# Performance work log

Measured on AMD Instinct MI355X. Metric: run time of the kernel, lower is better.

The kernel has to match this reference:

```python
import jax, jax.numpy as jnp
import numpy as np
import math

B, T, F_ = 4, 1024, 1024
TO_DIM, FROM_DIM, LATENT, H = 1024, 1024, 1024, 16
HEAD_DIM = LATENT // H

def _linear_params(key, in_dim, out_dim):
    kw, kb = jax.random.split(key)
    bound = 1.0 / math.sqrt(in_dim)
    W = jax.random.uniform(kw, (out_dim, in_dim), minval=-bound, maxval=bound, dtype=jnp.float32)
    b = jax.random.uniform(kb, (out_dim,), minval=-bound, maxval=bound, dtype=jnp.float32)
    return W, b

def setup_inputs() -> dict:
    key = jax.random.key(0)
    ks = jax.random.split(key, 7)
    X_to = jax.random.normal(ks[0], (B, T, TO_DIM), dtype=jnp.float32)
    X_from = jax.random.normal(ks[1], (B, F_, FROM_DIM), dtype=jnp.float32)
    mask_from = jax.random.randint(ks[2], (B, T, F_), 0, 2, dtype=jnp.int32)
    Wq, bq = _linear_params(ks[3], TO_DIM, LATENT)
    Wk, bk = _linear_params(ks[4], FROM_DIM, LATENT)
    Wv, bv = _linear_params(ks[5], FROM_DIM, LATENT)
    Wo, bo = _linear_params(ks[6], LATENT, TO_DIM)
    return {"X_to": X_to, "X_from": X_from, "mask_from": mask_from,
            "Wq": Wq, "bq": bq, "Wk": Wk, "bk": bk, "Wv": Wv, "bv": bv, "Wo": Wo, "bo": bo}

def _split_heads(x):
    # [b, t, (h k)] -> [b, h, t, k]
    b, t, _ = x.shape
    return x.reshape(b, t, H, HEAD_DIM).transpose(0, 2, 1, 3)

def reference(X_to, X_from, mask_from, Wq, bq, Wk, bk, Wv, bv, Wo, bo):
    Q = _split_heads(X_to @ Wq.T + bq)
    # NOTE: source swaps names — K comes from v_linear, V from k_linear. Reproduced literally.
    K = _split_heads(X_from @ Wv.T + bv)
    V = _split_heads(X_from @ Wk.T + bk)
    attn = jnp.einsum('bhtk,bhfk->bhtf', Q, K) / math.sqrt(HEAD_DIM)
    attn = jnp.where(mask_from[:, None, :, :] == 0, jnp.float32(-10000.0), attn)
    attn = jax.nn.softmax(attn, axis=-1)
    out = jnp.einsum('bhtf,bhfk->bhtk', attn, V)  # [b,h,t,k]
    out = out.transpose(0, 2, 1, 3).reshape(X_to.shape[0], X_to.shape[1], LATENT)
    return out @ Wo.T + bo
```

## Files before the change

### kernel.cpp

```cpp
#include <hip/hip_runtime.h>
#include <hip/hip_bf16.h>
#include <math.h>

#define BB 4
#define TT 1024
#define FF 1024
#define DIM 1024
#define NH 16
#define HD 64
#define MROWS (BB * TT)
#define FB (FF / 64)

typedef __attribute__((ext_vector_type(8))) short short8;
typedef __attribute__((ext_vector_type(4))) short short4v;
typedef __attribute__((ext_vector_type(4))) float f32x4;
typedef __hip_bfloat16 bf16;

__device__ __forceinline__ void async_copy16(const void* g, void* l) {
    __builtin_amdgcn_global_load_lds((const __attribute__((address_space(1))) void*)g,
                                     (__attribute__((address_space(3))) void*)l,
                                     16, 0, 0);
}

struct ConvArgs {
    const float* src[6];
    bf16* dst[6];
    int nvec[6];
    int blk_end[6];
    const int* mask;
    unsigned long long* Mb;
};

__global__ __launch_bounds__(256) void convert_pack(ConvArgs a) {
    int bx = blockIdx.x;
    if (bx >= a.blk_end[5]) {
        const int lane = threadIdx.x & 63;
        const int waveId = (bx - a.blk_end[5]) * 4 + (threadIdx.x >> 6);
#pragma unroll
        for (int it = 0; it < 16; ++it) {
            int c = waveId * 16 + it;
            int v = a.mask[(size_t)c * 64 + lane];
            unsigned long long bits = __ballot(v != 0);
            if (lane == 0) a.Mb[c] = bits;
        }
        return;
    }
    int seg = 0;
#pragma unroll
    for (int k = 0; k < 5; ++k) if (bx >= a.blk_end[k]) seg = k + 1;
    int b0 = seg ? a.blk_end[seg - 1] : 0;
    int idx = (bx - b0) * 256 + threadIdx.x;
    if (idx >= a.nvec[seg]) return;
    float4 v = ((const float4*)a.src[seg])[idx];
    union { bf16 t[4]; ushort4 u; } o;
    o.t[0] = __float2bfloat16(v.x);
    o.t[1] = __float2bfloat16(v.y);
    o.t[2] = __float2bfloat16(v.z);
    o.t[3] = __float2bfloat16(v.w);
    *(ushort4*)(a.dst[seg] + 4 * (size_t)idx) = o.u;
}

#define BK 64

struct QkvArgs {
    const bf16* A[3]; const bf16* W[3]; const float* bias[3]; bf16* C[3];
    int N[3]; int biasRow[3]; float scale[3];
};

#define BARRIER() __builtin_amdgcn_s_barrier()

__global__ __launch_bounds__(512) void gemm_qkv(QkvArgs q) {
    __shared__ bf16 lds[67584];

    const int op = blockIdx.y;
    const bf16* A = q.A[op];
    const bf16* W = q.W[op];
    const float* bias = q.bias[op];
    bf16* C = q.C[op];
    const int N = q.N[op];
    const int brow = q.biasRow[op];
    const float sc = q.scale[op];

    const int lin = blockIdx.x;
    const int xcd = lin & 7;
    const int t8  = lin >> 3;
    int mt, nt;
    if (brow) { mt = t8 & 3; nt = xcd * 2 + (t8 >> 2); }
    else      { mt = xcd * 2 + (t8 >> 2); nt = t8 & 3; }
    const int m0 = mt * 256, n0 = nt * 256;

    const int tid  = threadIdx.x;
    const int lane = tid & 63;
    const int wave = tid >> 6;
    const int quad = lane >> 4;
    const int l16  = lane & 15;
    const int wm   = wave >> 2;
    const int wn   = wave & 3;
    const int wbase = tid & ~63;

    const int srow = tid >> 3;
    const int scol = (tid & 7) ^ (srow & 7);
    const bf16* pA = A + (size_t)(m0 + srow) * DIM + scol * 8;
    const bf16* pB = W + (size_t)(n0 + srow) * DIM + scol * 8;

#define STAGE(P, ISB, TTL, HH) do { \
    const bf16* s_ = (P) + (size_t)(HH) * (128 * DIM) + (TTL) * 64; \
    bf16* d_ = lds + ((TTL) & 1) * 32768 + (ISB) * 16384 + (HH) * 8192 + wbase * 8; \
    async_copy16(s_, d_); \
    async_copy16(s_ + 64 * DIM, d_ + 4096); \
} while (0)

    f32x4 acc[8][4] = {};
    short8 a[4][2], b[4][2];

    STAGE(pA, 0, 0, 0); STAGE(pB, 1, 0, 0);
    STAGE(pA, 0, 0, 1); STAGE(pB, 1, 0, 1);
    STAGE(pA, 0, 1, 0); STAGE(pB, 1, 1, 0);
    asm volatile("s_waitcnt vmcnt(4)");
    BARRIER();

#define LDA(AH) do { \
    _Pragma("unroll") for (int miq = 0; miq < 4; ++miq) { \
        int r_ = (AH) * 128 + wm * 64 + miq * 16 + l16; \
        const bf16* ba_ = Ab + r_ * 64; \
        a[miq][0] = *(const short8*)(ba_ + ((quad ^ (r_ & 7)) * 8)); \
        a[miq][1] = *(const short8*)(ba_ + (((quad + 4) ^ (r_ & 7)) * 8)); \
    } } while (0)

#define LDB(BH) do { \
    _Pragma("unroll") for (int niq = 0; niq < 2; ++niq) { \
        int r_ = (BH) * 128 + wn * 32 + niq * 16 + l16; \
        const bf16* bb_ = Bb + r_ * 64; \
        b[(BH) * 2 + niq][0] = *(const short8*)(bb_ + ((quad ^ (r_ & 7)) * 8)); \
        b[(BH) * 2 + niq][1] = *(const short8*)(bb_ + (((quad + 4) ^ (r_ & 7)) * 8)); \
    } } while (0)

#define MMA(AH, BH) do { \
    _Pragma("unroll") for (int miq = 0; miq < 4; ++miq) \
    _Pragma("unroll") for (int niq = 0; niq < 2; ++niq) { \
        f32x4& c_ = acc[(AH) * 4 + miq][(BH) * 2 + niq]; \
        c_ = __builtin_amdgcn_mfma_f32_16x16x32_bf16(a[miq][0], b[(BH) * 2 + niq][0], c_, 0, 0, 0); \
        c_ = __builtin_amdgcn_mfma_f32_16x16x32_bf16(a[miq][1], b[(BH) * 2 + niq][1], c_, 0, 0, 0); \
    } } while (0)

#define PHASE_MFMA(AH, BH) do { \
    BARRIER(); \
    __builtin_amdgcn_s_setprio(1); \
    MMA(AH, BH); \
    __builtin_amdgcn_s_setprio(0); \
} while (0)

#pragma unroll 2
    for (int t = 0; t < 16; ++t) {
        const bf16* Ab = lds + (t & 1) * 32768;
        const bf16* Bb = Ab + 16384;

        LDA(0); LDB(0);
        if (t + 1 < 16) STAGE(pA, 0, t + 1, 1);
        PHASE_MFMA(0, 0);
        BARRIER();

        LDB(1);
        if (t + 1 < 16) STAGE(pB, 1, t + 1, 1);
        PHASE_MFMA(0, 1);
        BARRIER();

        LDA(1);
        if (t + 2 < 16) STAGE(pA, 0, t + 2, 0);
        PHASE_MFMA(1, 0);
        BARRIER();

        if (t + 2 < 16) STAGE(pB, 1, t + 2, 0);
        PHASE_MFMA(1, 1);
        if (t < 14)       { asm volatile("s_waitcnt vmcnt(4)"); }
        else if (t == 14) { asm volatile("s_waitcnt vmcnt(0)"); }
        BARRIER();
    }

    bf16* Cs = lds;
#pragma unroll
    for (int ni = 0; ni < 4; ++ni) {
        const int nl = (ni >> 1) * 128 + wn * 32 + (ni & 1) * 16 + l16;
        float bcol = brow ? 0.0f : bias[n0 + nl];
#pragma unroll
        for (int mi = 0; mi < 8; ++mi)
#pragma unroll
            for (int i = 0; i < 4; ++i) {
                const int ml = (mi >> 2) * 128 + wm * 64 + (mi & 3) * 16 + quad * 4 + i;
                float v = (acc[mi][ni][i] + (brow ? bias[m0 + ml] : bcol)) * sc;
                Cs[ml * 264 + nl] = __float2bfloat16(v);
            }
    }
    __syncthreads();
#pragma unroll
    for (int j = 0; j < 16; ++j) {
        int slot = j * 512 + tid;
        int rr = slot >> 5, cc = slot & 31;
        short8 v = *(const short8*)(Cs + rr * 264 + cc * 8);
        *(short8*)(C + (size_t)(m0 + rr) * N + n0 + cc * 8) = v;
    }
#undef STAGE
#undef LDA
#undef LDB
#undef MMA
#undef PHASE_MFMA
}

__global__ __launch_bounds__(256) void gemm_o(
    const bf16* __restrict__ A, const bf16* __restrict__ W,
    const float* __restrict__ bias, float* __restrict__ C)
{
    __shared__ float smemf[128 * 66];
    bf16* As = (bf16*)smemf;
    bf16* Bs = As + 128 * BK;

    const int lin = blockIdx.x + 16 * blockIdx.y;
    const int xcd = lin & 7;
    const int t   = lin >> 3;
    const int m0 = (xcd * 4 + (t >> 4)) * 128;
    const int n0 = (((t & 15) + 2 * xcd) & 15) * 64;

    const int tid  = threadIdx.x;
    const int lane = tid & 63;
    const int wave = tid >> 6;
    const int quad = lane >> 4;
    const int l16  = lane & 15;
    const int wm = wave & 1;
    const int wn = wave >> 1;
    const int wbase = tid & ~63;

    f32x4 acc[4][2] = {};

    for (int k0 = 0; k0 < DIM; k0 += BK) {
#pragma unroll
        for (int j = 0; j < 4; ++j) {
            int slot = j * 256 + tid;
            int r = slot >> 3;
            int g = (slot & 7) ^ (r & 7);
            async_copy16(A + (size_t)(m0 + r) * DIM + k0 + g * 8,
                         As + (size_t)(j * 256 + wbase) * 8);
        }
#pragma unroll
        for (int j = 0; j < 2; ++j) {
            int slot = j * 256 + tid;
            int r = slot >> 3;
            int g = (slot & 7) ^ (r & 7);
            async_copy16(W + (size_t)(n0 + r) * DIM + k0 + g * 8,
                         Bs + (size_t)(j * 256 + wbase) * 8);
        }
        __syncthreads();

#pragma unroll
        for (int kk = 0; kk < 2; ++kk) {
            short8 a[4], b[2];
#pragma unroll
            for (int mi = 0; mi < 4; ++mi) {
                int r = wm * 64 + mi * 16 + l16;
                int p = (kk * 4 + quad) ^ (r & 7);
                a[mi] = *(const short8*)(As + r * BK + p * 8);
            }
#pragma unroll
            for (int ni = 0; ni < 2; ++ni) {
                int r = wn * 32 + ni * 16 + l16;
                int p = (kk * 4 + quad) ^ (r & 7);
                b[ni] = *(const short8*)(Bs + r * BK + p * 8);
            }
#pragma unroll
            for (int mi = 0; mi < 4; ++mi)
#pragma unroll
                for (int ni = 0; ni < 2; ++ni)
                    acc[mi][ni] = __builtin_amdgcn_mfma_f32_16x16x32_bf16(
                        a[mi], b[ni], acc[mi][ni], 0, 0, 0);
        }
        __syncthreads();
    }

    float* Cs = smemf;
#pragma unroll
    for (int ni = 0; ni < 2; ++ni) {
        const int nl = wn * 32 + ni * 16 + l16;
        const float bcol = bias[n0 + nl];
#pragma unroll
        for (int mi = 0; mi < 4; ++mi)
#pragma unroll
            for (int i = 0; i < 4; ++i) {
                const int ml = wm * 64 + mi * 16 + quad * 4 + i;
                Cs[ml * 66 + nl] = acc[mi][ni][i] + bcol;
            }
    }
    __syncthreads();
#pragma unroll
    for (int j = 0; j < 8; ++j) {
        int slot = j * 256 + tid;
        int rr = slot >> 4, cc = slot & 15;
        float4 v = *(const float4*)(Cs + rr * 66 + cc * 4);
        *(float4*)(C + (size_t)(m0 + rr) * DIM + n0 + cc * 4) = v;
    }
}

__global__ __launch_bounds__(256, 3) void attn_kernel(
    const bf16* Qg, const bf16* __restrict__ Kg, const bf16* __restrict__ Vtg,
    const unsigned long long* __restrict__ Mbits, bf16* Og)
{
    __shared__ bf16 Ks[2 * 64 * 64];
    __shared__ bf16 Vts[2 * 64 * 64];
    __shared__ bf16 Pt[64 * 72];
    __shared__ float ls[64];

    const int tid  = threadIdx.x;
    const int lane = tid & 63;
    const int wave = tid >> 6;
    const int quad = lane >> 4;
    const int l16  = lane & 15;

    const int lin = blockIdx.x + 16 * (blockIdx.y + 16 * blockIdx.z);
    const int xcd = lin & 7;
    const int t   = lin >> 3;
    const int bh  = xcd * 8 + (t >> 4);
    const int b   = bh >> 4;
    const int h   = bh & 15;
    const int t0  = (t & 15) * 64;

    const size_t qrow0 = (size_t)b * TT + t0;
    const size_t krow0 = (size_t)b * FF;
    const int wbase = tid & ~63;
    const int myrow = wave * 16 + l16;

    const bf16* qptr = Qg + (qrow0 + myrow) * DIM + h * HD;
    short8 qb0 = *(const short8*)(qptr + quad * 8);
    short8 qb1 = *(const short8*)(qptr + 32 + quad * 8);

    const int srow = tid >> 3;
    const int sg   = ((tid & 7) ^ (srow & 7)) * 8;
    const bf16* kS = Kg + (krow0 + srow) * DIM + h * HD + sg;
    const bf16* vS = Vtg + (size_t)(h * HD + srow) * MROWS + b * FF + sg;

#define STAGE_KV(BUF, IT) do { \
    const bf16* ks_ = kS + (size_t)((IT) * 64) * DIM; \
    const bf16* vs_ = vS + (IT) * 64; \
    bf16* kd_ = Ks + (BUF) * 4096 + wbase * 8; \
    bf16* vd_ = Vts + (BUF) * 4096 + wbase * 8; \
    async_copy16(ks_, kd_); \
    async_copy16(ks_ + (size_t)32 * DIM, kd_ + 2048); \
    async_copy16(vs_, vd_); \
    async_copy16(vs_ + (size_t)32 * MROWS, vd_ + 2048); \
} while (0)

    const unsigned long long* mrow = Mbits + (qrow0 + myrow) * FB;
    unsigned long long w = mrow[0];

    float lsum = 0.f;
    f32x4 oacc[4] = {};

    STAGE_KV(0, 0);
    STAGE_KV(1, 1);
    asm volatile("s_waitcnt vmcnt(4)");
    BARRIER();

#pragma unroll 2
    for (int it = 0; it < 16; ++it) {
        const bf16* Kc = Ks + (it & 1) * 4096;
        const bf16* Vc = Vts + (it & 1) * 4096;

        unsigned long long nw = (it < 15) ? mrow[it + 1] : 0;

        f32x4 sacc[4];
        __builtin_amdgcn_s_setprio(1);
#pragma unroll
        for (int ft = 0; ft < 4; ++ft) {
            int r = ft * 16 + l16;
            short8 ka0 = *(const short8*)(Kc + r * 64 + ((quad       ^ (r & 7)) * 8));
            short8 ka1 = *(const short8*)(Kc + r * 64 + (((quad + 4) ^ (r & 7)) * 8));
            f32x4 s = {};
            s = __builtin_amdgcn_mfma_f32_16x16x32_bf16(ka0, qb0, s, 0, 0, 0);
            s = __builtin_amdgcn_mfma_f32_16x16x32_bf16(ka1, qb1, s, 0, 0, 0);
            sacc[ft] = s;
        }
        __builtin_amdgcn_s_setprio(0);

#pragma unroll
        for (int ft = 0; ft < 4; ++ft) {
            const unsigned bits4 =
                (unsigned)(w >> (ft * 16 + quad * 4)) & 0xFu;
            union { short4v v; short s[4]; } pk;
            float psum = 0.f;
#pragma unroll
            for (int i = 0; i < 4; ++i) {
                float p = (bits4 >> i) & 1u ? __expf(sacc[ft][i]) : 0.f;
                psum += p;
                pk.s[i] = (short)__bfloat16_as_ushort(__float2bfloat16(p));
            }
            lsum += psum;
            *(short4v*)(Pt + myrow * 72 + ft * 16 + quad * 4) = pk.v;
        }
        w = nw;

        short8 pa[2];
        pa[0] = *(const short8*)(Pt + myrow * 72 + quad * 8);
        pa[1] = *(const short8*)(Pt + myrow * 72 + 32 + quad * 8);
        __builtin_amdgcn_s_setprio(1);
#pragma unroll
        for (int nt = 0; nt < 4; ++nt) {
            int rd = nt * 16 + l16;
#pragma unroll
            for (int kf = 0; kf < 2; ++kf) {
                int g = (kf * 4 + quad) ^ (rd & 7);
                short8 vb = *(const short8*)(Vc + rd * 64 + g * 8);
                oacc[nt] = __builtin_amdgcn_mfma_f32_16x16x32_bf16(pa[kf], vb, oacc[nt], 0, 0, 0);
            }
        }
        __builtin_amdgcn_s_setprio(0);

        BARRIER();
        if (it + 2 < 16) STAGE_KV(it & 1, it + 2);
        if (it < 14)       { asm volatile("s_waitcnt vmcnt(4)"); }
        else if (it == 14) { asm volatile("s_waitcnt vmcnt(0)"); }
        BARRIER();
    }
#undef STAGE_KV

    lsum += __shfl_xor(lsum, 16);
    lsum += __shfl_xor(lsum, 32);
    if (quad == 0) ls[myrow] = lsum;

#pragma unroll
    for (int i = 0; i < 4; ++i) {
        float inv = 1.0f / ls[wave * 16 + quad * 4 + i];
        const int prow = wave * 16 + quad * 4 + i;
#pragma unroll
        for (int nt = 0; nt < 4; ++nt)
            Pt[prow * 72 + nt * 16 + l16] = __float2bfloat16(oacc[nt][i] * inv);
    }
    __syncthreads();
#pragma unroll
    for (int j = 0; j < 2; ++j) {
        int s = j * 256 + tid;
        int rr = s >> 3, off = (s & 7) * 8;
        short8 v = *(const short8*)(Pt + rr * 72 + off);
        *(short8*)(Og + (qrow0 + rr) * DIM + h * HD + off) = v;
    }
}

extern "C" void kernel_launch(void* const* d_in, const int* in_sizes, int n_in,
                              void* d_out, int out_size, void* d_ws, size_t ws_size,
                              hipStream_t stream) {
    const float* X_to   = (const float*)d_in[0];
    const float* X_from = (const float*)d_in[1];
    const int*   mask   = (const int*)  d_in[2];
    const float* Wq     = (const float*)d_in[3];
    const float* bq     = (const float*)d_in[4];
    const float* Wk     = (const float*)d_in[5];
    const float* bk     = (const float*)d_in[6];
    const float* Wv     = (const float*)d_in[7];
    const float* bv     = (const float*)d_in[8];
    const float* Wo     = (const float*)d_in[9];
    const float* bo     = (const float*)d_in[10];
    float* out = (float*)d_out;

    char* ws = (char*)d_ws;
    bf16* Xt16 = (bf16*)(ws);
    bf16* Xf16 = (bf16*)(ws + (8u  << 20));
    bf16* Wq16 = (bf16*)(ws + (16u << 20));
    bf16* Wv16 = (bf16*)(ws + (18u << 20));
    bf16* Wk16 = (bf16*)(ws + (20u << 20));
    bf16* Wo16 = (bf16*)(ws + (22u << 20));
    bf16* Q16  = (bf16*)(ws + (24u << 20));
    bf16* K16  = (bf16*)(ws + (32u << 20));
    bf16* Vt16 = (bf16*)(ws + (40u << 20));
    unsigned long long* Mb = (unsigned long long*)(ws + (48u << 20));

    ConvArgs ca;
    ca.src[0] = X_to;   ca.dst[0] = Xt16; ca.nvec[0] = MROWS * DIM / 4;
    ca.src[1] = X_from; ca.dst[1] = Xf16; ca.nvec[1] = MROWS * DIM / 4;
    ca.src[2] = Wq;     ca.dst[2] = Wq16; ca.nvec[2] = DIM * DIM / 4;
    ca.src[3] = Wv;     ca.dst[3] = Wv16; ca.nvec[3] = DIM * DIM / 4;
    ca.src[4] = Wk;     ca.dst[4] = Wk16; ca.nvec[4] = DIM * DIM / 4;
    ca.src[5] = Wo;     ca.dst[5] = Wo16; ca.nvec[5] = DIM * DIM / 4;
    int cum = 0;
    for (int k = 0; k < 6; ++k) { cum += ca.nvec[k] / 256; ca.blk_end[k] = cum; }
    ca.mask = mask; ca.Mb = Mb;
    convert_pack<<<cum + 1024, 256, 0, stream>>>(ca);

    QkvArgs qa;
    qa.A[0] = Xt16; qa.W[0] = Wq16; qa.bias[0] = bq; qa.C[0] = Q16;
    qa.N[0] = DIM; qa.biasRow[0] = 0; qa.scale[0] = 0.125f;
    qa.A[1] = Xf16; qa.W[1] = Wv16; qa.bias[1] = bv; qa.C[1] = K16;
    qa.N[1] = DIM; qa.biasRow[1] = 0; qa.scale[1] = 1.0f;
    qa.A[2] = Wk16; qa.W[2] = Xf16; qa.bias[2] = bk; qa.C[2] = Vt16;
    qa.N[2] = MROWS; qa.biasRow[2] = 1; qa.scale[2] = 1.0f;
    gemm_qkv<<<dim3(64, 3), 512, 0, stream>>>(qa);

    attn_kernel<<<dim3(TT / 64, NH, BB), 256, 0, stream>>>(
        Q16, K16, Vt16, Mb, Q16);

    gemm_o<<<dim3(DIM / 64, MROWS / 128), 256, 0, stream>>>(Q16, Wo16, bo, out);
}
```

Measured before the change: 225.2 us.

## Shrink QKV GEMM tiles to 128x128 and double-buffer the output GEMM

```diff
diff --git a/kernel.cpp b/kernel.cpp
--- a/kernel.cpp
+++ b/kernel.cpp
@@ -21,6 +21,8 @@
                                      (__attribute__((address_space(3))) void*)l,
                                      16, 0, 0);
 }
+
+#define BARRIER() __builtin_amdgcn_s_barrier()
 
 struct ConvArgs {
     const float* src[6];
@@ -67,12 +69,10 @@
     int N[3]; int biasRow[3]; float scale[3];
 };
 
-#define BARRIER() __builtin_amdgcn_s_barrier()
-
-__global__ __launch_bounds__(512) void gemm_qkv(QkvArgs q) {
-    __shared__ bf16 lds[67584];
-
-    const int op = blockIdx.y;
+__global__ __launch_bounds__(256, 2) void gemm_qkv(QkvArgs q) {
+    __shared__ bf16 lds[32768];
+
+    const int op = blockIdx.z;
     const bf16* A = q.A[op];
     const bf16* W = q.W[op];
     const float* bias = q.bias[op];
@@ -81,144 +81,17 @@
     const int brow = q.biasRow[op];
     const float sc = q.scale[op];
 
-    const int lin = blockIdx.x;
+    const int lin = blockIdx.x + 8 * blockIdx.y;
     const int xcd = lin & 7;
     const int t8  = lin >> 3;
-    int mt, nt;
-    if (brow) { mt = t8 & 3; nt = xcd * 2 + (t8 >> 2); }
-    else      { mt = xcd * 2 + (t8 >> 2); nt = t8 & 3; }
-    const int m0 = mt * 256, n0 = nt * 256;
-
-    const int tid  = threadIdx.x;
-    const int lane = tid & 63;
-    const int wave = tid >> 6;
-    const int quad = lane >> 4;
-    const int l16  = lane & 15;
-    const int wm   = wave >> 2;
-    const int wn   = wave & 3;
-    const int wbase = tid & ~63;
-
-    const int srow = tid >> 3;
-    const int scol = (tid & 7) ^ (srow & 7);
-    const bf16* pA = A + (size_t)(m0 + srow) * DIM + scol * 8;
-    const bf16* pB = W + (size_t)(n0 + srow) * DIM + scol * 8;
-
-#define STAGE(P, ISB, TTL, HH) do { \
-    const bf16* s_ = (P) + (size_t)(HH) * (128 * DIM) + (TTL) * 64; \
-    bf16* d_ = lds + ((TTL) & 1) * 32768 + (ISB) * 16384 + (HH) * 8192 + wbase * 8; \
-    async_copy16(s_, d_); \
-    async_copy16(s_ + 64 * DIM, d_ + 4096); \
-} while (0)
-
-    f32x4 acc[8][4] = {};
-    short8 a[4][2], b[4][2];
-
-    STAGE(pA, 0, 0, 0); STAGE(pB, 1, 0, 0);
-    STAGE(pA, 0, 0, 1); STAGE(pB, 1, 0, 1);
-    STAGE(pA, 0, 1, 0); STAGE(pB, 1, 1, 0);
-    asm volatile("s_waitcnt vmcnt(4)");
-    BARRIER();
-
-#define LDA(AH) do { \
-    _Pragma("unroll") for (int miq = 0; miq < 4; ++miq) { \
-        int r_ = (AH) * 128 + wm * 64 + miq * 16 + l16; \
-        const bf16* ba_ = Ab + r_ * 64; \
-        a[miq][0] = *(const short8*)(ba_ + ((quad ^ (r_ & 7)) * 8)); \
-        a[miq][1] = *(const short8*)(ba_ + (((quad + 4) ^ (r_ & 7)) * 8)); \
-    } } while (0)
-
-#define LDB(BH) do { \
-    _Pragma("unroll") for (int niq = 0; niq < 2; ++niq) { \
-        int r_ = (BH) * 128 + wn * 32 + niq * 16 + l16; \
-        const bf16* bb_ = Bb + r_ * 64; \
-        b[(BH) * 2 + niq][0] = *(const short8*)(bb_ + ((quad ^ (r_ & 7)) * 8)); \
-        b[(BH) * 2 + niq][1] = *(const short8*)(bb_ + (((quad + 4) ^ (r_ & 7)) * 8)); \
-    } } while (0)
-
-#define MMA(AH, BH) do { \
-    _Pragma("unroll") for (int miq = 0; miq < 4; ++miq) \
-    _Pragma("unroll") for (int niq = 0; niq < 2; ++niq) { \
-        f32x4& c_ = acc[(AH) * 4 + miq][(BH) * 2 + niq]; \
-        c_ = __builtin_amdgcn_mfma_f32_16x16x32_bf16(a[miq][0], b[(BH) * 2 + niq][0], c_, 0, 0, 0); \
-        c_ = __builtin_amdgcn_mfma_f32_16x16x32_bf16(a[miq][1], b[(BH) * 2 + niq][1], c_, 0, 0, 0); \
-    } } while (0)
-
-#define PHASE_MFMA(AH, BH) do { \
-    BARRIER(); \
-    __builtin_amdgcn_s_setprio(1); \
-    MMA(AH, BH); \
-    __builtin_amdgcn_s_setprio(0); \
-} while (0)
-
-#pragma unroll 2
-    for (int t = 0; t < 16; ++t) {
-        const bf16* Ab = lds + (t & 1) * 32768;
-        const bf16* Bb = Ab + 16384;
-
-        LDA(0); LDB(0);
-        if (t + 1 < 16) STAGE(pA, 0, t + 1, 1);
-        PHASE_MFMA(0, 0);
-        BARRIER();
-
-        LDB(1);
-        if (t + 1 < 16) STAGE(pB, 1, t + 1, 1);
-        PHASE_MFMA(0, 1);
-        BARRIER();
-
-        LDA(1);
-        if (t + 2 < 16) STAGE(pA, 0, t + 2, 0);
-        PHASE_MFMA(1, 0);
-        BARRIER();
-
-        if (t + 2 < 16) STAGE(pB, 1, t + 2, 0);
-        PHASE_MFMA(1, 1);
-        if (t < 14)       { asm volatile("s_waitcnt vmcnt(4)"); }
-        else if (t == 14) { asm volatile("s_waitcnt vmcnt(0)"); }
-        BARRIER();
-    }
-
-    bf16* Cs = lds;
-#pragma unroll
-    for (int ni = 0; ni < 4; ++ni) {
-        const int nl = (ni >> 1) * 128 + wn * 32 + (ni & 1) * 16 + l16;
-        float bcol = brow ? 0.0f : bias[n0 + nl];
-#pragma unroll
-        for (int mi = 0; mi < 8; ++mi)
-#pragma unroll
-            for (int i = 0; i < 4; ++i) {
-                const int ml = (mi >> 2) * 128 + wm * 64 + (mi & 3) * 16 + quad * 4 + i;
-                float v = (acc[mi][ni][i] + (brow ? bias[m0 + ml] : bcol)) * sc;
-                Cs[ml * 264 + nl] = __float2bfloat16(v);
-            }
-    }
-    __syncthreads();
-#pragma unroll
-    for (int j = 0; j < 16; ++j) {
-        int slot = j * 512 + tid;
-        int rr = slot >> 5, cc = slot & 31;
-        short8 v = *(const short8*)(Cs + rr * 264 + cc * 8);
-        *(short8*)(C + (size_t)(m0 + rr) * N + n0 + cc * 8) = v;
-    }
-#undef STAGE
-#undef LDA
-#undef LDB
-#undef MMA
-#undef PHASE_MFMA
-}
-
-__global__ __launch_bounds__(256) void gemm_o(
-    const bf16* __restrict__ A, const bf16* __restrict__ W,
-    const float* __restrict__ bias, float* __restrict__ C)
-{
-    __shared__ float smemf[128 * 66];
-    bf16* As = (bf16*)smemf;
-    bf16* Bs = As + 128 * BK;
-
-    const int lin = blockIdx.x + 16 * blockIdx.y;
-    const int xcd = lin & 7;
-    const int t   = lin >> 3;
-    const int m0 = (xcd * 4 + (t >> 4)) * 128;
-    const int n0 = (((t & 15) + 2 * xcd) & 15) * 64;
+    int m0, n0;
+    if (brow) {
+        m0 = (((t8 & 7) + xcd) & 7) * 128;
+        n0 = (xcd * 4 + (t8 >> 3)) * 128;
+    } else {
+        m0 = (xcd * 4 + (t8 >> 3)) * 128;
+        n0 = (((t8 & 7) + xcd) & 7) * 128;
+    }
 
     const int tid  = threadIdx.x;
     const int lane = tid & 63;
@@ -229,53 +102,174 @@
     const int wn = wave >> 1;
     const int wbase = tid & ~63;
 
-    f32x4 acc[4][2] = {};
-
-    for (int k0 = 0; k0 < DIM; k0 += BK) {
-#pragma unroll
-        for (int j = 0; j < 4; ++j) {
-            int slot = j * 256 + tid;
-            int r = slot >> 3;
-            int g = (slot & 7) ^ (r & 7);
-            async_copy16(A + (size_t)(m0 + r) * DIM + k0 + g * 8,
-                         As + (size_t)(j * 256 + wbase) * 8);
-        }
-#pragma unroll
-        for (int j = 0; j < 2; ++j) {
-            int slot = j * 256 + tid;
-            int r = slot >> 3;
-            int g = (slot & 7) ^ (r & 7);
-            async_copy16(W + (size_t)(n0 + r) * DIM + k0 + g * 8,
-                         Bs + (size_t)(j * 256 + wbase) * 8);
-        }
-        __syncthreads();
-
+    const int srow = tid >> 3;
+    const int scol = (tid & 7) ^ (srow & 7);
+    const bf16* pA = A + (size_t)(m0 + srow) * DIM + scol * 8;
+    const bf16* pB = W + (size_t)(n0 + srow) * DIM + scol * 8;
+
+#define STAGE(T) do { \
+    const bf16* sa_ = pA + (size_t)(T) * 64; \
+    const bf16* sb_ = pB + (size_t)(T) * 64; \
+    bf16* base_ = lds + ((T) & 1) * 16384; \
+    _Pragma("unroll") for (int j = 0; j < 4; ++j) { \
+        async_copy16(sa_ + (size_t)(j * 32) * DIM, base_ + (j * 256 + wbase) * 8); \
+        async_copy16(sb_ + (size_t)(j * 32) * DIM, base_ + 8192 + (j * 256 + wbase) * 8); \
+    } \
+} while (0)
+
+    f32x4 acc[4][4] = {};
+
+    STAGE(0); STAGE(1);
+    asm volatile("s_waitcnt vmcnt(8)");
+    BARRIER();
+
+#pragma unroll 2
+    for (int t = 0; t < 16; ++t) {
+        const bf16* As = lds + (t & 1) * 16384;
+        const bf16* Bs = As + 8192;
+
+        short8 a2[2][4], b2[2][4];
 #pragma unroll
         for (int kk = 0; kk < 2; ++kk) {
-            short8 a[4], b[2];
 #pragma unroll
             for (int mi = 0; mi < 4; ++mi) {
                 int r = wm * 64 + mi * 16 + l16;
                 int p = (kk * 4 + quad) ^ (r & 7);
-                a[mi] = *(const short8*)(As + r * BK + p * 8);
+                a2[kk][mi] = *(const short8*)(As + r * 64 + p * 8);
+            }
+#pragma unroll
+            for (int ni = 0; ni < 4; ++ni) {
+                int r = wn * 64 + ni * 16 + l16;
+                int p = (kk * 4 + quad) ^ (r & 7);
+                b2[kk][ni] = *(const short8*)(Bs + r * 64 + p * 8);
+            }
+        }
+        __builtin_amdgcn_s_setprio(1);
+#pragma unroll
+        for (int kk = 0; kk < 2; ++kk)
+#pragma unroll
+            for (int mi = 0; mi < 4; ++mi)
+#pragma unroll
+                for (int ni = 0; ni < 4; ++ni)
+                    acc[mi][ni] = __builtin_amdgcn_mfma_f32_16x16x32_bf16(
+                        a2[kk][mi], b2[kk][ni], acc[mi][ni], 0, 0, 0);
+        __builtin_amdgcn_s_setprio(0);
+
+        BARRIER();
+        if (t + 2 < 16) STAGE(t + 2);
+        if (t < 14)       { asm volatile("s_waitcnt vmcnt(8)"); }
+        else if (t == 14) { asm volatile("s_waitcnt vmcnt(0)"); }
+        BARRIER();
+    }
+
+    bf16* Cs = lds;
+#pragma unroll
+    for (int ni = 0; ni < 4; ++ni) {
+        const int nl = wn * 64 + ni * 16 + l16;
+        float bcol = brow ? 0.0f : bias[n0 + nl];
+#pragma unroll
+        for (int mi = 0; mi < 4; ++mi)
+#pragma unroll
+            for (int i = 0; i < 4; ++i) {
+                const int ml = wm * 64 + mi * 16 + quad * 4 + i;
+                float v = (acc[mi][ni][i] + (brow ? bias[m0 + ml] : bcol)) * sc;
+                Cs[ml * 132 + nl] = __float2bfloat16(v);
+            }
+    }
+    __syncthreads();
+#pragma unroll
+    for (int j = 0; j < 8; ++j) {
+        int slot = j * 256 + tid;
+        int rr = slot >> 4, cc = slot & 15;
+        short8 v = *(const short8*)(Cs + rr * 132 + cc * 8);
+        *(short8*)(C + (size_t)(m0 + rr) * N + n0 + cc * 8) = v;
+    }
+#undef STAGE
+}
+
+__global__ __launch_bounds__(256, 2) void gemm_o(
+    const bf16* __restrict__ A, const bf16* __restrict__ W,
+    const float* __restrict__ bias, float* __restrict__ C)
+{
+    __shared__ bf16 lds[24576];
+
+    const int lin = blockIdx.x + 16 * blockIdx.y;
+    const int xcd = lin & 7;
+    const int t8  = lin >> 3;
+    const int m0 = (xcd * 4 + (t8 >> 4)) * 128;
+    const int n0 = (((t8 & 15) + 2 * xcd) & 15) * 64;
+
+    const int tid  = threadIdx.x;
+    const int lane = tid & 63;
+    const int wave = tid >> 6;
+    const int quad = lane >> 4;
+    const int l16  = lane & 15;
+    const int wm = wave & 1;
+    const int wn = wave >> 1;
+    const int wbase = tid & ~63;
+
+    const int srow = tid >> 3;
+    const int scol = (tid & 7) ^ (srow & 7);
+    const bf16* pA = A + (size_t)(m0 + srow) * DIM + scol * 8;
+    const bf16* pB = W + (size_t)(n0 + srow) * DIM + scol * 8;
+
+#define STAGE_O(T) do { \
+    const bf16* sa_ = pA + (size_t)(T) * 64; \
+    const bf16* sb_ = pB + (size_t)(T) * 64; \
+    bf16* ab_ = lds + ((T) & 1) * 8192; \
+    bf16* bb_ = lds + 16384 + ((T) & 1) * 4096; \
+    _Pragma("unroll") for (int j = 0; j < 4; ++j) \
+        async_copy16(sa_ + (size_t)(j * 32) * DIM, ab_ + (j * 256 + wbase) * 8); \
+    _Pragma("unroll") for (int j = 0; j < 2; ++j) \
+        async_copy16(sb_ + (size_t)(j * 32) * DIM, bb_ + (j * 256 + wbase) * 8); \
+} while (0)
+
+    f32x4 acc[4][2] = {};
+
+    STAGE_O(0); STAGE_O(1);
+    asm volatile("s_waitcnt vmcnt(6)");
+    BARRIER();
+
+#pragma unroll 2
+    for (int t = 0; t < 16; ++t) {
+        const bf16* As = lds + (t & 1) * 8192;
+        const bf16* Bs = lds + 16384 + (t & 1) * 4096;
+
+        short8 a2[2][4], b2[2][2];
+#pragma unroll
+        for (int kk = 0; kk < 2; ++kk) {
+#pragma unroll
+            for (int mi = 0; mi < 4; ++mi) {
+                int r = wm * 64 + mi * 16 + l16;
+                int p = (kk * 4 + quad) ^ (r & 7);
+                a2[kk][mi] = *(const short8*)(As + r * 64 + p * 8);
             }
 #pragma unroll
             for (int ni = 0; ni < 2; ++ni) {
                 int r = wn * 32 + ni * 16 + l16;
                 int p = (kk * 4 + quad) ^ (r & 7);
-                b[ni] = *(const short8*)(Bs + r * BK + p * 8);
-            }
+                b2[kk][ni] = *(const short8*)(Bs + r * 64 + p * 8);
+            }
+        }
+        __builtin_amdgcn_s_setprio(1);
+#pragma unroll
+        for (int kk = 0; kk < 2; ++kk)
 #pragma unroll
             for (int mi = 0; mi < 4; ++mi)
 #pragma unroll
                 for (int ni = 0; ni < 2; ++ni)
                     acc[mi][ni] = __builtin_amdgcn_mfma_f32_16x16x32_bf16(
-                        a[mi], b[ni], acc[mi][ni], 0, 0, 0);
-        }
-        __syncthreads();
-    }
-
-    float* Cs = smemf;
+                        a2[kk][mi], b2[kk][ni], acc[mi][ni], 0, 0, 0);
+        __builtin_amdgcn_s_setprio(0);
+
+        BARRIER();
+        if (t + 2 < 16) STAGE_O(t + 2);
+        if (t < 14)       { asm volatile("s_waitcnt vmcnt(6)"); }
+        else if (t == 14) { asm volatile("s_waitcnt vmcnt(0)"); }
+        BARRIER();
+    }
+
+    float* Cs = (float*)lds;
 #pragma unroll
     for (int ni = 0; ni < 2; ++ni) {
         const int nl = wn * 32 + ni * 16 + l16;
@@ -296,6 +290,7 @@
         float4 v = *(const float4*)(Cs + rr * 66 + cc * 4);
         *(float4*)(C + (size_t)(m0 + rr) * DIM + n0 + cc * 4) = v;
     }
+#undef STAGE_O
 }
 
 __global__ __launch_bounds__(256, 3) void attn_kernel(
@@ -488,7 +483,7 @@
     qa.N[1] = DIM; qa.biasRow[1] = 0; qa.scale[1] = 1.0f;
     qa.A[2] = Wk16; qa.W[2] = Xf16; qa.bias[2] = bk; qa.C[2] = Vt16;
     qa.N[2] = MROWS; qa.biasRow[2] = 1; qa.scale[2] = 1.0f;
-    gemm_qkv<<<dim3(64, 3), 512, 0, stream>>>(qa);
+    gemm_qkv<<<dim3(8, 32, 3), 256, 0, stream>>>(qa);
 
     attn_kernel<<<dim3(TT / 64, NH, BB), 256, 0, stream>>>(
         Q16, K16, Vt16, Mb, Q16);
```

Measured after the change: 219.5 us. 1.03x faster.
